# Optimization experiments

Hardware: AMD Instinct MI355X
Metric: run time of the kernel (lower is better)

Reference implementation:

```python
import jax, jax.numpy as jnp
import numpy as np

B, ENC, DEC, TSTEPS, PRED = 512, 2048, 1024, 12, 24
IN_DIM = ENC + 1 + TSTEPS  # 2061


def setup_inputs() -> dict:
    key = jax.random.key(0)
    ks = jax.random.split(key, 12)
    s = 0.05  # small init scale for numerical stability
    return {
        "encoder_out": jax.random.normal(ks[0], (B, ENC), jnp.float32),
        "oni_input": jax.random.normal(ks[1], (B, 1), jnp.float32),
        "ssi": jax.random.normal(ks[2], (B, TSTEPS), jnp.float32),
        "W_ih": jax.random.normal(ks[3], (4 * DEC, IN_DIM), jnp.float32) * s,
        "b_ih": jax.random.normal(ks[4], (4 * DEC,), jnp.float32) * s,
        "W_hh": jax.random.normal(ks[5], (4 * DEC, DEC), jnp.float32) * s,
        "b_hh": jax.random.normal(ks[6], (4 * DEC,), jnp.float32) * s,
        "W_l1": jax.random.normal(ks[7], (DEC, DEC * PRED), jnp.float32) * s,
        "b_l1": jax.random.normal(ks[8], (DEC,), jnp.float32) * s,
        "W_l2": jax.random.normal(ks[9], (DEC, DEC), jnp.float32) * s,
        "b_l2": jax.random.normal(ks[10], (DEC,), jnp.float32) * s,
    }


def reference(encoder_out, oni_input, ssi, W_ih, b_ih, W_hh, b_hh, W_l1, b_l1, W_l2, b_l2):
    # cfg.lstm=True, cfg.loss_criterion='enso', dropout p=0 (identity)
    x = jnp.concatenate([encoder_out, oni_input, ssi], axis=1)  # (B, IN_DIM)
    # input is identical every step: precompute input projection once
    x_proj = x @ W_ih.T + b_ih + b_hh  # (B, 4*DEC)
    D = W_hh.shape[1]
    T = W_l1.shape[1] // D
    b = x.shape[0]

    def step(carry, _):
        h, c = carry
        gates = x_proj + h @ W_hh.T  # (B, 4D), PyTorch gate order i,f,g,o
        i, f, g, o = jnp.split(gates, 4, axis=1)
        c = jax.nn.sigmoid(f) * c + jax.nn.sigmoid(i) * jnp.tanh(g)
        h = jax.nn.sigmoid(o) * jnp.tanh(c)
        return (h, c), h

    init = (jnp.zeros((b, D), x.dtype), jnp.zeros((b, D), x.dtype))
    _, hs = jax.lax.scan(step, init, None, length=T)  # (T, B, D)
    # torch.stack(dim=2) then flatten(start_dim=1) -> layout (B, D*T)
    preds = jnp.transpose(hs, (1, 2, 0)).reshape(b, D * T)
    preds = jax.nn.sigmoid(preds @ W_l1.T + b_l1)
    preds = preds @ W_l2.T + b_l2
    return jax.nn.sigmoid(preds)  # 'enso' head; dropout(p=0) is identity
```

## Files before the change

kernel.cpp:

```cpp
#include <hip/hip_runtime.h>
#include <hip/hip_bf16.h>

#define BSZ   512
#define ENCD  2048
#define DECD  1024
#define TST   12
#define PREDT 24
#define INDIM 2061
#define KPAD  2112
#define G4    4096
#define KH    24576

typedef __attribute__((ext_vector_type(8))) short s8v;
typedef __attribute__((ext_vector_type(4))) short s4v;
typedef __attribute__((ext_vector_type(4))) float f4v;

__device__ __forceinline__ short bf16_of(float f) {
  union { float f; unsigned u; } x; x.f = f;
  unsigned r = x.u + 0x7fffu + ((x.u >> 16) & 1u);
  return (short)(r >> 16);
}
__device__ __forceinline__ float sigf(float x) { return 1.f / (1.f + __expf(-x)); }
__device__ __forceinline__ float tanh_(float x) { return 1.f - 2.f / (1.f + __expf(2.f * x)); }

__device__ __forceinline__ int lds_off(int row, int colb) {
  return row * 128 + (colb ^ ((row & 7) << 4));
}


__global__ void prep_x(const float* __restrict__ enc, const float* __restrict__ oni,
                       const float* __restrict__ ssi, short* __restrict__ x_bf) {
  int idx = blockIdx.x * 256 + threadIdx.x;
  if (idx >= BSZ * KPAD) return;
  int b = idx / KPAD, k = idx % KPAD;
  float v = 0.f;
  if (k < ENCD) v = enc[b * ENCD + k];
  else if (k == ENCD) v = oni[b];
  else if (k < INDIM) v = ssi[b * TST + (k - ENCD - 1)];
  x_bf[idx] = bf16_of(v);
}

__global__ void prep_wih(const float* __restrict__ W, short* __restrict__ o) {
  int idx = blockIdx.x * 256 + threadIdx.x;
  int rp = idx / KPAD; int k = idx - rp * KPAD;
  int dblk = rp >> 6, rem = rp & 63, g = rem >> 4, dl = rem & 15;
  int srow = g * 1024 + dblk * 16 + dl;
  float v = (k < INDIM) ? W[(size_t)srow * INDIM + k] : 0.f;
  o[idx] = bf16_of(v);
}

__global__ void prep_whh(const float* __restrict__ W, short* __restrict__ o) {
  int idx = blockIdx.x * 256 + threadIdx.x;
  int rp = idx >> 10; int k = idx & 1023;
  int dblk = rp >> 6, rem = rp & 63, g = rem >> 4, dl = rem & 15;
  int srow = g * 1024 + dblk * 16 + dl;
  o[idx] = bf16_of(W[(size_t)srow * 1024 + k]);
}

__global__ __launch_bounds__(256, 1) void xproj_k(
    const short* __restrict__ x_bf, const short* __restrict__ wih_bf,
    const float* __restrict__ b_ih, const float* __restrict__ b_hh,
    float* __restrict__ xp_p) {
  __shared__ __align__(16) char sA[2][16384];
  __shared__ __align__(16) char sB[2][8192];
  int tid = threadIdx.x, lane = tid & 63, w = tid >> 6;
  int L = blockIdx.x;
  int bm = L >> 6, pb = (L & 7) * 8 + ((L >> 3) & 7);
  const int l4 = lane & 15, lg = lane >> 4;

  s8v aR[4], bR[2];
  auto LOAD = [&](int kt) {
    int kk = kt * 64;
#pragma unroll
    for (int i = 0; i < 4; ++i) {
      int c = tid + i * 256, r = c >> 3, sl = c & 7;
      aR[i] = *(const s8v*)(x_bf + (size_t)(bm * 128 + r) * KPAD + kk + sl * 8);
    }
#pragma unroll
    for (int i = 0; i < 2; ++i) {
      int c = tid + i * 256, r = c >> 3, sl = c & 7;
      bR[i] = *(const s8v*)(wih_bf + (size_t)(pb * 64 + r) * KPAD + kk + sl * 8);
    }
  };
  auto WRITE = [&](int buf) {
#pragma unroll
    for (int i = 0; i < 4; ++i) {
      int c = tid + i * 256, r = c >> 3, sl = c & 7;
      *(s8v*)(sA[buf] + lds_off(r, sl * 16)) = aR[i];
    }
#pragma unroll
    for (int i = 0; i < 2; ++i) {
      int c = tid + i * 256, r = c >> 3, sl = c & 7;
      *(s8v*)(sB[buf] + lds_off(r, sl * 16)) = bR[i];
    }
  };

  f4v acc[2][4] = {};
  LOAD(0); WRITE(0); LOAD(1);
  __syncthreads();
  for (int kt = 0; kt < 33; ++kt) {
    int cur = kt & 1;
    if (kt < 32) WRITE(cur ^ 1);
    if (kt < 31) LOAD(kt + 2);
#pragma unroll
    for (int ks = 0; ks < 2; ++ks) {
      int colb = ks * 64 + lg * 16;
      s8v af[2], bf[4];
#pragma unroll
      for (int mi = 0; mi < 2; ++mi)
        af[mi] = *(const s8v*)(sA[cur] + lds_off(w * 32 + mi * 16 + l4, colb));
#pragma unroll
      for (int ni = 0; ni < 4; ++ni)
        bf[ni] = *(const s8v*)(sB[cur] + lds_off(ni * 16 + l4, colb));
#pragma unroll
      for (int mi = 0; mi < 2; ++mi)
#pragma unroll
        for (int ni = 0; ni < 4; ++ni)
          acc[mi][ni] = __builtin_amdgcn_mfma_f32_16x16x32_bf16(af[mi], bf[ni], acc[mi][ni], 0, 0, 0);
    }
    __syncthreads();
  }
#pragma unroll
  for (int ni = 0; ni < 4; ++ni) {
    int src = ni * 1024 + pb * 16 + l4;
    float bv = b_ih[src] + b_hh[src];
#pragma unroll
    for (int mi = 0; mi < 2; ++mi)
#pragma unroll
      for (int j = 0; j < 4; ++j) {
        int row = bm * 128 + w * 32 + mi * 16 + lg * 4 + j;
        xp_p[(size_t)row * G4 + pb * 64 + ni * 16 + l4] = acc[mi][ni][j] + bv;
      }
  }
}

template <bool FIRST>
__global__ __launch_bounds__(256, 2) void step_k(
    const short* __restrict__ h_in, const short* __restrict__ whh_bf,
    const float* __restrict__ xp_p, float* __restrict__ c_st,
    short* __restrict__ h_out, short* __restrict__ hs_t, int tstep) {
  __shared__ __align__(16) char sB[2][8192];
  __shared__ __align__(16) char sA[4][2][4096];
  int tid = threadIdx.x, lane = tid & 63, w = tid >> 6;
  int cp = blockIdx.x, bm = blockIdx.y;
  const int l4 = lane & 15, lg = lane >> 4;
  const int d = cp * 16 + l4;

  float xg[2][4][4], cpre[2][4];
#pragma unroll
  for (int mi = 0; mi < 2; ++mi)
#pragma unroll
    for (int j = 0; j < 4; ++j) {
      int row = bm * 128 + w * 32 + mi * 16 + lg * 4 + j;
      size_t xb = (size_t)row * G4 + cp * 64 + l4;
      xg[mi][j][0] = xp_p[xb];
      xg[mi][j][1] = xp_p[xb + 16];
      xg[mi][j][2] = xp_p[xb + 32];
      xg[mi][j][3] = xp_p[xb + 48];
      cpre[mi][j] = FIRST ? 0.f : c_st[(size_t)row * DECD + d];
    }

  f4v acc[2][4] = {};

  if (!FIRST) {
    const short* bbase = whh_bf + (size_t)cp * 64 * DECD;
    const short* abase = h_in + (size_t)(bm * 128 + w * 32) * DECD;
    s8v aR[4], bR[2];
    auto LOAD = [&](int kt) {
      int kk = kt * 64;
#pragma unroll
      for (int i = 0; i < 4; ++i) {
        int c = lane + i * 64, r = c >> 3, sl = c & 7;
        aR[i] = *(const s8v*)(abase + (size_t)r * DECD + kk + sl * 8);
      }
#pragma unroll
      for (int i = 0; i < 2; ++i) {
        int c = tid + i * 256, r = c >> 3, sl = c & 7;
        bR[i] = *(const s8v*)(bbase + (size_t)r * DECD + kk + sl * 8);
      }
    };
    auto WRITE = [&](int buf) {
#pragma unroll
      for (int i = 0; i < 4; ++i) {
        int c = lane + i * 64, r = c >> 3, sl = c & 7;
        *(s8v*)(sA[w][buf] + lds_off(r, sl * 16)) = aR[i];
      }
#pragma unroll
      for (int i = 0; i < 2; ++i) {
        int c = tid + i * 256, r = c >> 3, sl = c & 7;
        *(s8v*)(sB[buf] + lds_off(r, sl * 16)) = bR[i];
      }
    };
    LOAD(0); WRITE(0); LOAD(1);
    __syncthreads();
    for (int kt = 0; kt < 16; ++kt) {
      int cur = kt & 1;
      if (kt < 15) WRITE(cur ^ 1);
      if (kt < 14) LOAD(kt + 2);
#pragma unroll
      for (int ks = 0; ks < 2; ++ks) {
        int colb = ks * 64 + lg * 16;
        s8v af[2], bf[4];
#pragma unroll
        for (int mi = 0; mi < 2; ++mi)
          af[mi] = *(const s8v*)(sA[w][cur] + lds_off(mi * 16 + l4, colb));
#pragma unroll
        for (int ni = 0; ni < 4; ++ni)
          bf[ni] = *(const s8v*)(sB[cur] + lds_off(ni * 16 + l4, colb));
#pragma unroll
        for (int mi = 0; mi < 2; ++mi)
#pragma unroll
          for (int ni = 0; ni < 4; ++ni)
            acc[mi][ni] = __builtin_amdgcn_mfma_f32_16x16x32_bf16(af[mi], bf[ni], acc[mi][ni], 0, 0, 0);
      }
      __syncthreads();
    }
  }

#pragma unroll
  for (int mi = 0; mi < 2; ++mi)
#pragma unroll
    for (int j = 0; j < 4; ++j) {
      int row = bm * 128 + w * 32 + mi * 16 + lg * 4 + j;
      float gi = xg[mi][j][0] + acc[mi][0][j];
      float gf = xg[mi][j][1] + acc[mi][1][j];
      float gg = xg[mi][j][2] + acc[mi][2][j];
      float go = xg[mi][j][3] + acc[mi][3][j];
      float cn = sigf(gf) * cpre[mi][j] + sigf(gi) * tanh_(gg);
      float h = sigf(go) * tanh_(cn);
      size_t cd = (size_t)row * DECD + d;
      c_st[cd] = cn;
      short hb = bf16_of(h);
      if (tstep < 23) h_out[cd] = hb;
      hs_t[(size_t)tstep * (BSZ * DECD) + cd] = hb;
    }
}

__global__ void transpose_k(const short* __restrict__ hs_t, short* __restrict__ hs) {
  int g = blockIdx.x * 256 + threadIdx.x;
  int row = g >> 10, d = g & 1023;
#pragma unroll
  for (int i = 0; i < 3; ++i) {
    s8v v;
#pragma unroll
    for (int u = 0; u < 8; ++u)
      v[u] = hs_t[(size_t)(i * 8 + u) * (BSZ * DECD) + (size_t)row * DECD + d];
    *(s8v*)(hs + (size_t)row * KH + d * PREDT + i * 8) = v;
  }
}

template <int EPI>
__global__ __launch_bounds__(256, 2) void gemm2_k(
    const short* __restrict__ A, int lda, const float* __restrict__ Bw, int ldb,
    int ntiles, int kchunk, const float* __restrict__ bias1,
    float* __restrict__ Cf, int ldc) {
  __shared__ __align__(16) char sA[2][16384];
  __shared__ __align__(16) char sB[2][16384];
  int tid = threadIdx.x, lane = tid & 63, wid = tid >> 6;
  int wr = wid >> 1, wc = wid & 1, l4 = lane & 15, lg = lane >> 4;
  int bn = blockIdx.x * 128, bm = blockIdx.y * 128;
  int k0 = blockIdx.z * kchunk;
  size_t zoff = (size_t)blockIdx.z * BSZ * (size_t)ldc;
  s8v aR[4]; f4v bR[4][2];
  auto LOAD = [&](int kt) {
    int kk = k0 + kt * 64;
#pragma unroll
    for (int i = 0; i < 4; ++i) {
      int c = tid + i * 256, r = c >> 3, sl = c & 7;
      aR[i] = *(const s8v*)(A + (size_t)(bm + r) * lda + kk + sl * 8);
      const float* src = Bw + (size_t)(bn + r) * ldb + kk + sl * 8;
      bR[i][0] = *(const f4v*)src;
      bR[i][1] = *(const f4v*)(src + 4);
    }
  };
  auto WRITE = [&](int buf) {
#pragma unroll
    for (int i = 0; i < 4; ++i) {
      int c = tid + i * 256, r = c >> 3, sl = c & 7;
      *(s8v*)(sA[buf] + lds_off(r, sl * 16)) = aR[i];
      s8v v;
#pragma unroll
      for (int j = 0; j < 4; ++j) { v[j] = bf16_of(bR[i][0][j]); v[4 + j] = bf16_of(bR[i][1][j]); }
      *(s8v*)(sB[buf] + lds_off(r, sl * 16)) = v;
    }
  };
  f4v acc[4][4] = {};
  LOAD(0); WRITE(0);
  if (ntiles > 1) LOAD(1);
  __syncthreads();
  for (int kt = 0; kt < ntiles; ++kt) {
    int cur = kt & 1;
    if (kt + 1 < ntiles) WRITE(cur ^ 1);
    if (kt + 2 < ntiles) LOAD(kt + 2);
#pragma unroll
    for (int ks = 0; ks < 2; ++ks) {
      int colb = ks * 64 + lg * 16;
      s8v af[4], bf[4];
#pragma unroll
      for (int mi = 0; mi < 4; ++mi)
        af[mi] = *(const s8v*)(sA[cur] + lds_off(wr * 64 + mi * 16 + l4, colb));
#pragma unroll
      for (int ni = 0; ni < 4; ++ni)
        bf[ni] = *(const s8v*)(sB[cur] + lds_off(wc * 64 + ni * 16 + l4, colb));
#pragma unroll
      for (int mi = 0; mi < 4; ++mi)
#pragma unroll
        for (int ni = 0; ni < 4; ++ni)
          acc[mi][ni] = __builtin_amdgcn_mfma_f32_16x16x32_bf16(af[mi], bf[ni], acc[mi][ni], 0, 0, 0);
    }
    __syncthreads();
  }
#pragma unroll
  for (int mi = 0; mi < 4; ++mi)
#pragma unroll
    for (int ni = 0; ni < 4; ++ni)
#pragma unroll
      for (int j = 0; j < 4; ++j) {
        int row = bm + wr * 64 + mi * 16 + lg * 4 + j;
        int col = bn + wc * 64 + ni * 16 + l4;
        float v = acc[mi][ni][j];
        if (EPI == 1) Cf[zoff + (size_t)row * ldc + col] = v;
        else Cf[(size_t)row * ldc + col] = sigf(v + bias1[col]);
      }
}

__global__ void reduce16(const float* __restrict__ part, const float* __restrict__ b_l1,
                         short* __restrict__ z1) {
  int i4 = blockIdx.x * 256 + threadIdx.x;
  int base = i4 * 4;
  int n = base & (DECD - 1);
  f4v s = *(const f4v*)(b_l1 + n);
#pragma unroll
  for (int z = 0; z < 16; ++z) {
    f4v p = *(const f4v*)(part + (size_t)z * (BSZ * DECD) + base);
#pragma unroll
    for (int j = 0; j < 4; ++j) s[j] += p[j];
  }
  s4v o;
#pragma unroll
  for (int j = 0; j < 4; ++j) o[j] = bf16_of(sigf(s[j]));
  *(s4v*)(z1 + base) = o;
}


extern "C" void kernel_launch(void* const* d_in, const int* in_sizes, int n_in,
                              void* d_out, int out_size, void* d_ws, size_t ws_size,
                              hipStream_t stream) {
  const float* enc  = (const float*)d_in[0];
  const float* oni  = (const float*)d_in[1];
  const float* ssi  = (const float*)d_in[2];
  const float* W_ih = (const float*)d_in[3];
  const float* b_ih = (const float*)d_in[4];
  const float* W_hh = (const float*)d_in[5];
  const float* b_hh = (const float*)d_in[6];
  const float* W_l1 = (const float*)d_in[7];
  const float* b_l1 = (const float*)d_in[8];
  const float* W_l2 = (const float*)d_in[9];
  const float* b_l2 = (const float*)d_in[10];
  float* out = (float*)d_out;
  (void)in_sizes; (void)n_in; (void)out_size; (void)ws_size;

  char* ws = (char*)d_ws;
  size_t off = 0;
  auto carve = [&](size_t bytes) { char* p = ws + off; off += (bytes + 255) & ~(size_t)255; return p; };
  short* x_bf   = (short*)carve((size_t)BSZ * KPAD * 2);
  short* wih_bf = (short*)carve((size_t)G4 * KPAD * 2);
  short* whh_bf = (short*)carve((size_t)G4 * DECD * 2);
  float* xp_p   = (float*)carve((size_t)BSZ * G4 * 4);
  short* h0     = (short*)carve((size_t)BSZ * DECD * 2);
  short* h1     = (short*)carve((size_t)BSZ * DECD * 2);
  float* c_st   = (float*)carve((size_t)BSZ * DECD * 4);
  float* part   = (float*)ws;
  if (off < (size_t)16 * BSZ * DECD * 4) off = (((size_t)16 * BSZ * DECD * 4) + 255) & ~(size_t)255;
  short* hs_t   = (short*)carve((size_t)PREDT * BSZ * DECD * 2);
  short* hs     = (short*)carve((size_t)BSZ * KH * 2);
  short* z1     = (short*)carve((size_t)BSZ * DECD * 2);

  prep_x  <<<(BSZ * KPAD) / 256, 256, 0, stream>>>(enc, oni, ssi, x_bf);
  prep_wih<<<(G4 * KPAD) / 256, 256, 0, stream>>>(W_ih, wih_bf);
  prep_whh<<<(G4 * DECD) / 256, 256, 0, stream>>>(W_hh, whh_bf);

  xproj_k<<<256, 256, 0, stream>>>(x_bf, wih_bf, b_ih, b_hh, xp_p);

  step_k<true><<<dim3(64, 4), 256, 0, stream>>>(nullptr, whh_bf, xp_p, c_st, h0, hs_t, 0);
  for (int t = 1; t < PREDT; ++t) {
    short* hr = (t & 1) ? h0 : h1;
    short* hw = (t & 1) ? h1 : h0;
    step_k<false><<<dim3(64, 4), 256, 0, stream>>>(hr, whh_bf, xp_p, c_st, hw, hs_t, t);
  }

  transpose_k<<<(BSZ * DECD) / 256, 256, 0, stream>>>(hs_t, hs);

  gemm2_k<1><<<dim3(8, 4, 16), 256, 0, stream>>>(hs, KH, W_l1, KH, 24, KH / 16, nullptr, part, DECD);
  reduce16<<<(BSZ * DECD) / 1024, 256, 0, stream>>>(part, b_l1, z1);

  gemm2_k<2><<<dim3(8, 4, 1), 256, 0, stream>>>(z1, DECD, W_l2, DECD, 16, DECD, b_l2, out, DECD);
}
```

Measured before the change: 412.6 us.

## Fuse W_ih conversion into xproj, write hs directly, shrink GEMM M tile

Removes the separate prep_wih kernel: xproj now reads fp32 W_ih directly with row remapping and converts to bf16 in registers, zero-padding past the input dimension. The step kernel writes hidden states straight into the interleaved (B, D*T) layout, which removes the hs_t buffer and the transpose kernel. The final GEMMs use a 64-row M tile with launch bounds allowing 3 blocks, doubling grid size for better occupancy. The trade-offs are scattered 2-byte strided stores in each step kernel and redundant fp32 weight reads and conversion in xproj.

New measurement: 487.5 us. 18.2% more time.

```diff
diff --git a/kernel.cpp b/kernel.cpp
--- a/kernel.cpp
+++ b/kernel.cpp
@@ -40,15 +40,6 @@
   x_bf[idx] = bf16_of(v);
 }
 
-__global__ void prep_wih(const float* __restrict__ W, short* __restrict__ o) {
-  int idx = blockIdx.x * 256 + threadIdx.x;
-  int rp = idx / KPAD; int k = idx - rp * KPAD;
-  int dblk = rp >> 6, rem = rp & 63, g = rem >> 4, dl = rem & 15;
-  int srow = g * 1024 + dblk * 16 + dl;
-  float v = (k < INDIM) ? W[(size_t)srow * INDIM + k] : 0.f;
-  o[idx] = bf16_of(v);
-}
-
 __global__ void prep_whh(const float* __restrict__ W, short* __restrict__ o) {
   int idx = blockIdx.x * 256 + threadIdx.x;
   int rp = idx >> 10; int k = idx & 1023;
@@ -58,7 +49,7 @@
 }
 
 __global__ __launch_bounds__(256, 1) void xproj_k(
-    const short* __restrict__ x_bf, const short* __restrict__ wih_bf,
+    const short* __restrict__ x_bf, const float* __restrict__ W_ih,
     const float* __restrict__ b_ih, const float* __restrict__ b_hh,
     float* __restrict__ xp_p) {
   __shared__ __align__(16) char sA[2][16384];
@@ -79,7 +70,20 @@
 #pragma unroll
     for (int i = 0; i < 2; ++i) {
       int c = tid + i * 256, r = c >> 3, sl = c & 7;
-      bR[i] = *(const s8v*)(wih_bf + (size_t)(pb * 64 + r) * KPAD + kk + sl * 8);
+      int srow = (r >> 4) * 1024 + pb * 16 + (r & 15);
+      const float* src = W_ih + (size_t)srow * INDIM + kk + sl * 8;
+      if (kt < 32) {
+        f4v f0 = *(const f4v*)src;
+        f4v f1 = *(const f4v*)(src + 4);
+#pragma unroll
+        for (int j = 0; j < 4; ++j) { bR[i][j] = bf16_of(f0[j]); bR[i][4 + j] = bf16_of(f1[j]); }
+      } else {
+#pragma unroll
+        for (int j = 0; j < 8; ++j) {
+          int kg = kk + sl * 8 + j;
+          bR[i][j] = (kg < INDIM) ? bf16_of(src[j]) : (short)0;
+        }
+      }
     }
   };
   auto WRITE = [&](int buf) {
@@ -138,7 +142,7 @@
 __global__ __launch_bounds__(256, 2) void step_k(
     const short* __restrict__ h_in, const short* __restrict__ whh_bf,
     const float* __restrict__ xp_p, float* __restrict__ c_st,
-    short* __restrict__ h_out, short* __restrict__ hs_t, int tstep) {
+    short* __restrict__ h_out, short* __restrict__ hs, int tstep) {
   __shared__ __align__(16) char sB[2][8192];
   __shared__ __align__(16) char sA[4][2][4096];
   int tid = threadIdx.x, lane = tid & 63, w = tid >> 6;
@@ -232,42 +236,33 @@
       c_st[cd] = cn;
       short hb = bf16_of(h);
       if (tstep < 23) h_out[cd] = hb;
-      hs_t[(size_t)tstep * (BSZ * DECD) + cd] = hb;
-    }
-}
-
-__global__ void transpose_k(const short* __restrict__ hs_t, short* __restrict__ hs) {
-  int g = blockIdx.x * 256 + threadIdx.x;
-  int row = g >> 10, d = g & 1023;
-#pragma unroll
-  for (int i = 0; i < 3; ++i) {
-    s8v v;
-#pragma unroll
-    for (int u = 0; u < 8; ++u)
-      v[u] = hs_t[(size_t)(i * 8 + u) * (BSZ * DECD) + (size_t)row * DECD + d];
-    *(s8v*)(hs + (size_t)row * KH + d * PREDT + i * 8) = v;
-  }
+      hs[(size_t)row * KH + d * PREDT + tstep] = hb;
+    }
 }
 
 template <int EPI>
-__global__ __launch_bounds__(256, 2) void gemm2_k(
+__global__ __launch_bounds__(256, 3) void gemm3_k(
     const short* __restrict__ A, int lda, const float* __restrict__ Bw, int ldb,
     int ntiles, int kchunk, const float* __restrict__ bias1,
     float* __restrict__ Cf, int ldc) {
-  __shared__ __align__(16) char sA[2][16384];
+  __shared__ __align__(16) char sA[2][8192];
   __shared__ __align__(16) char sB[2][16384];
   int tid = threadIdx.x, lane = tid & 63, wid = tid >> 6;
   int wr = wid >> 1, wc = wid & 1, l4 = lane & 15, lg = lane >> 4;
-  int bn = blockIdx.x * 128, bm = blockIdx.y * 128;
+  int bn = blockIdx.x * 128, bm = blockIdx.y * 64;
   int k0 = blockIdx.z * kchunk;
   size_t zoff = (size_t)blockIdx.z * BSZ * (size_t)ldc;
-  s8v aR[4]; f4v bR[4][2];
+  s8v aR[2]; f4v bR[4][2];
   auto LOAD = [&](int kt) {
     int kk = k0 + kt * 64;
 #pragma unroll
+    for (int i = 0; i < 2; ++i) {
+      int c = tid + i * 256, r = c >> 3, sl = c & 7;
+      aR[i] = *(const s8v*)(A + (size_t)(bm + r) * lda + kk + sl * 8);
+    }
+#pragma unroll
     for (int i = 0; i < 4; ++i) {
       int c = tid + i * 256, r = c >> 3, sl = c & 7;
-      aR[i] = *(const s8v*)(A + (size_t)(bm + r) * lda + kk + sl * 8);
       const float* src = Bw + (size_t)(bn + r) * ldb + kk + sl * 8;
       bR[i][0] = *(const f4v*)src;
       bR[i][1] = *(const f4v*)(src + 4);
@@ -275,16 +270,20 @@
   };
   auto WRITE = [&](int buf) {
 #pragma unroll
+    for (int i = 0; i < 2; ++i) {
+      int c = tid + i * 256, r = c >> 3, sl = c & 7;
+      *(s8v*)(sA[buf] + lds_off(r, sl * 16)) = aR[i];
+    }
+#pragma unroll
     for (int i = 0; i < 4; ++i) {
       int c = tid + i * 256, r = c >> 3, sl = c & 7;
-      *(s8v*)(sA[buf] + lds_off(r, sl * 16)) = aR[i];
       s8v v;
 #pragma unroll
       for (int j = 0; j < 4; ++j) { v[j] = bf16_of(bR[i][0][j]); v[4 + j] = bf16_of(bR[i][1][j]); }
       *(s8v*)(sB[buf] + lds_off(r, sl * 16)) = v;
     }
   };
-  f4v acc[4][4] = {};
+  f4v acc[2][4] = {};
   LOAD(0); WRITE(0);
   if (ntiles > 1) LOAD(1);
   __syncthreads();
@@ -295,15 +294,15 @@
 #pragma unroll
     for (int ks = 0; ks < 2; ++ks) {
       int colb = ks * 64 + lg * 16;
-      s8v af[4], bf[4];
-#pragma unroll
-      for (int mi = 0; mi < 4; ++mi)
-        af[mi] = *(const s8v*)(sA[cur] + lds_off(wr * 64 + mi * 16 + l4, colb));
+      s8v af[2], bf[4];
+#pragma unroll
+      for (int mi = 0; mi < 2; ++mi)
+        af[mi] = *(const s8v*)(sA[cur] + lds_off(wr * 32 + mi * 16 + l4, colb));
 #pragma unroll
       for (int ni = 0; ni < 4; ++ni)
         bf[ni] = *(const s8v*)(sB[cur] + lds_off(wc * 64 + ni * 16 + l4, colb));
 #pragma unroll
-      for (int mi = 0; mi < 4; ++mi)
+      for (int mi = 0; mi < 2; ++mi)
 #pragma unroll
         for (int ni = 0; ni < 4; ++ni)
           acc[mi][ni] = __builtin_amdgcn_mfma_f32_16x16x32_bf16(af[mi], bf[ni], acc[mi][ni], 0, 0, 0);
@@ -311,12 +310,12 @@
     __syncthreads();
   }
 #pragma unroll
-  for (int mi = 0; mi < 4; ++mi)
+  for (int mi = 0; mi < 2; ++mi)
 #pragma unroll
     for (int ni = 0; ni < 4; ++ni)
 #pragma unroll
       for (int j = 0; j < 4; ++j) {
-        int row = bm + wr * 64 + mi * 16 + lg * 4 + j;
+        int row = bm + wr * 32 + mi * 16 + lg * 4 + j;
         int col = bn + wc * 64 + ni * 16 + l4;
         float v = acc[mi][ni][j];
         if (EPI == 1) Cf[zoff + (size_t)row * ldc + col] = v;
@@ -364,7 +363,6 @@
   size_t off = 0;
   auto carve = [&](size_t bytes) { char* p = ws + off; off += (bytes + 255) & ~(size_t)255; return p; };
   short* x_bf   = (short*)carve((size_t)BSZ * KPAD * 2);
-  short* wih_bf = (short*)carve((size_t)G4 * KPAD * 2);
   short* whh_bf = (short*)carve((size_t)G4 * DECD * 2);
   float* xp_p   = (float*)carve((size_t)BSZ * G4 * 4);
   short* h0     = (short*)carve((size_t)BSZ * DECD * 2);
@@ -372,27 +370,23 @@
   float* c_st   = (float*)carve((size_t)BSZ * DECD * 4);
   float* part   = (float*)ws;
   if (off < (size_t)16 * BSZ * DECD * 4) off = (((size_t)16 * BSZ * DECD * 4) + 255) & ~(size_t)255;
-  short* hs_t   = (short*)carve((size_t)PREDT * BSZ * DECD * 2);
   short* hs     = (short*)carve((size_t)BSZ * KH * 2);
   short* z1     = (short*)carve((size_t)BSZ * DECD * 2);
 
   prep_x  <<<(BSZ * KPAD) / 256, 256, 0, stream>>>(enc, oni, ssi, x_bf);
-  prep_wih<<<(G4 * KPAD) / 256, 256, 0, stream>>>(W_ih, wih_bf);
   prep_whh<<<(G4 * DECD) / 256, 256, 0, stream>>>(W_hh, whh_bf);
 
-  xproj_k<<<256, 256, 0, stream>>>(x_bf, wih_bf, b_ih, b_hh, xp_p);
-
-  step_k<true><<<dim3(64, 4), 256, 0, stream>>>(nullptr, whh_bf, xp_p, c_st, h0, hs_t, 0);
+  xproj_k<<<256, 256, 0, stream>>>(x_bf, W_ih, b_ih, b_hh, xp_p);
+
+  step_k<true><<<dim3(64, 4), 256, 0, stream>>>(nullptr, whh_bf, xp_p, c_st, h0, hs, 0);
   for (int t = 1; t < PREDT; ++t) {
     short* hr = (t & 1) ? h0 : h1;
     short* hw = (t & 1) ? h1 : h0;
-    step_k<false><<<dim3(64, 4), 256, 0, stream>>>(hr, whh_bf, xp_p, c_st, hw, hs_t, t);
-  }
-
-  transpose_k<<<(BSZ * DECD) / 256, 256, 0, stream>>>(hs_t, hs);
-
-  gemm2_k<1><<<dim3(8, 4, 16), 256, 0, stream>>>(hs, KH, W_l1, KH, 24, KH / 16, nullptr, part, DECD);
+    step_k<false><<<dim3(64, 4), 256, 0, stream>>>(hr, whh_bf, xp_p, c_st, hw, hs, t);
+  }
+
+  gemm3_k<1><<<dim3(8, 8, 16), 256, 0, stream>>>(hs, KH, W_l1, KH, 24, KH / 16, nullptr, part, DECD);
   reduce16<<<(BSZ * DECD) / 1024, 256, 0, stream>>>(part, b_l1, z1);
 
-  gemm2_k<2><<<dim3(8, 4, 1), 256, 0, stream>>>(z1, DECD, W_l2, DECD, 16, DECD, b_l2, out, DECD);
-}
+  gemm3_k<2><<<dim3(8, 8, 1), 256, 0, stream>>>(z1, DECD, W_l2, DECD, 16, DECD, b_l2, out, DECD);
+}
```

## Fuse W_ih conversion into xproj and overlap W_l1 bf16 conversion with LSTM steps

Applied to the files above, without the earlier changes.

Drops the separate prep_wih kernel: xproj now reads fp32 W_ih directly, converts it to bf16 in registers and handles the K-tail with guarded loads. The 24 latency-bound LSTM step launches each get an extra row of blocks that converts a slice of W_l1 to bf16, hiding that conversion inside steps that leave the GPU underused. The large GEMM then reads bf16 weights, halving its weight traffic. The h ping-pong buffers are removed and steps read the previous h from hs_t. This costs extra workspace, with a fallback path when the workspace is too small, and adds unaligned float4 loads on W_ih rows since the row stride of 2061 is odd.

After: 507.1 us. 1.23x slower.

```diff
diff --git a/kernel.cpp b/kernel.cpp
--- a/kernel.cpp
+++ b/kernel.cpp
@@ -40,15 +40,6 @@
   x_bf[idx] = bf16_of(v);
 }
 
-__global__ void prep_wih(const float* __restrict__ W, short* __restrict__ o) {
-  int idx = blockIdx.x * 256 + threadIdx.x;
-  int rp = idx / KPAD; int k = idx - rp * KPAD;
-  int dblk = rp >> 6, rem = rp & 63, g = rem >> 4, dl = rem & 15;
-  int srow = g * 1024 + dblk * 16 + dl;
-  float v = (k < INDIM) ? W[(size_t)srow * INDIM + k] : 0.f;
-  o[idx] = bf16_of(v);
-}
-
 __global__ void prep_whh(const float* __restrict__ W, short* __restrict__ o) {
   int idx = blockIdx.x * 256 + threadIdx.x;
   int rp = idx >> 10; int k = idx & 1023;
@@ -58,7 +49,7 @@
 }
 
 __global__ __launch_bounds__(256, 1) void xproj_k(
-    const short* __restrict__ x_bf, const short* __restrict__ wih_bf,
+    const short* __restrict__ x_bf, const float* __restrict__ W_ih,
     const float* __restrict__ b_ih, const float* __restrict__ b_hh,
     float* __restrict__ xp_p) {
   __shared__ __align__(16) char sA[2][16384];
@@ -79,7 +70,20 @@
 #pragma unroll
     for (int i = 0; i < 2; ++i) {
       int c = tid + i * 256, r = c >> 3, sl = c & 7;
-      bR[i] = *(const s8v*)(wih_bf + (size_t)(pb * 64 + r) * KPAD + kk + sl * 8);
+      int srow = (r >> 4) * 1024 + pb * 16 + (r & 15);
+      const float* src = W_ih + (size_t)srow * INDIM + kk + sl * 8;
+      if (kt < 32) {
+        f4v f0 = *(const f4v*)src;
+        f4v f1 = *(const f4v*)(src + 4);
+#pragma unroll
+        for (int j = 0; j < 4; ++j) { bR[i][j] = bf16_of(f0[j]); bR[i][4 + j] = bf16_of(f1[j]); }
+      } else {
+#pragma unroll
+        for (int j = 0; j < 8; ++j) {
+          int kg = kk + sl * 8 + j;
+          bR[i][j] = (kg < INDIM) ? bf16_of(src[j]) : (short)0;
+        }
+      }
     }
   };
   auto WRITE = [&](int buf) {
@@ -134,14 +138,29 @@
   }
 }
 
-template <bool FIRST>
+template <bool FIRST, bool CONV>
 __global__ __launch_bounds__(256, 2) void step_k(
-    const short* __restrict__ h_in, const short* __restrict__ whh_bf,
-    const float* __restrict__ xp_p, float* __restrict__ c_st,
-    short* __restrict__ h_out, short* __restrict__ hs_t, int tstep) {
+    const short* __restrict__ whh_bf, const float* __restrict__ xp_p,
+    float* __restrict__ c_st, short* __restrict__ hs_t, int tstep,
+    const float* __restrict__ wl1, short* __restrict__ wl1b) {
   __shared__ __align__(16) char sB[2][8192];
   __shared__ __align__(16) char sA[4][2][4096];
   int tid = threadIdx.x, lane = tid & 63, w = tid >> 6;
+
+  if (CONV && blockIdx.y == 4) {
+    size_t base = (size_t)tstep * 1048576 + (size_t)(blockIdx.x * 256 + tid) * 64;
+#pragma unroll
+    for (int i = 0; i < 8; ++i) {
+      f4v f0 = *(const f4v*)(wl1 + base + i * 8);
+      f4v f1 = *(const f4v*)(wl1 + base + i * 8 + 4);
+      s8v v;
+#pragma unroll
+      for (int j = 0; j < 4; ++j) { v[j] = bf16_of(f0[j]); v[4 + j] = bf16_of(f1[j]); }
+      *(s8v*)(wl1b + base + i * 8) = v;
+    }
+    return;
+  }
+
   int cp = blockIdx.x, bm = blockIdx.y;
   const int l4 = lane & 15, lg = lane >> 4;
   const int d = cp * 16 + l4;
@@ -163,6 +182,7 @@
   f4v acc[2][4] = {};
 
   if (!FIRST) {
+    const short* h_in = hs_t + (size_t)(tstep - 1) * (BSZ * DECD);
     const short* bbase = whh_bf + (size_t)cp * 64 * DECD;
     const short* abase = h_in + (size_t)(bm * 128 + w * 32) * DECD;
     s8v aR[4], bR[2];
@@ -217,6 +237,7 @@
     }
   }
 
+  short* hw = hs_t + (size_t)tstep * (BSZ * DECD);
 #pragma unroll
   for (int mi = 0; mi < 2; ++mi)
 #pragma unroll
@@ -230,9 +251,7 @@
       float h = sigf(go) * tanh_(cn);
       size_t cd = (size_t)row * DECD + d;
       c_st[cd] = cn;
-      short hb = bf16_of(h);
-      if (tstep < 23) h_out[cd] = hb;
-      hs_t[(size_t)tstep * (BSZ * DECD) + cd] = hb;
+      hw[cd] = bf16_of(h);
     }
 }
 
@@ -249,9 +268,10 @@
   }
 }
 
-template <int EPI>
+template <int EPI, bool BF16B>
 __global__ __launch_bounds__(256, 2) void gemm2_k(
-    const short* __restrict__ A, int lda, const float* __restrict__ Bw, int ldb,
+    const short* __restrict__ A, int lda, const short* __restrict__ Bb,
+    const float* __restrict__ Bf, int ldb,
     int ntiles, int kchunk, const float* __restrict__ bias1,
     float* __restrict__ Cf, int ldc) {
   __shared__ __align__(16) char sA[2][16384];
@@ -261,16 +281,20 @@
   int bn = blockIdx.x * 128, bm = blockIdx.y * 128;
   int k0 = blockIdx.z * kchunk;
   size_t zoff = (size_t)blockIdx.z * BSZ * (size_t)ldc;
-  s8v aR[4]; f4v bR[4][2];
+  s8v aR[4], bB[4]; f4v bR[4][2];
   auto LOAD = [&](int kt) {
     int kk = k0 + kt * 64;
 #pragma unroll
     for (int i = 0; i < 4; ++i) {
       int c = tid + i * 256, r = c >> 3, sl = c & 7;
       aR[i] = *(const s8v*)(A + (size_t)(bm + r) * lda + kk + sl * 8);
-      const float* src = Bw + (size_t)(bn + r) * ldb + kk + sl * 8;
-      bR[i][0] = *(const f4v*)src;
-      bR[i][1] = *(const f4v*)(src + 4);
+      if (BF16B) {
+        bB[i] = *(const s8v*)(Bb + (size_t)(bn + r) * ldb + kk + sl * 8);
+      } else {
+        const float* src = Bf + (size_t)(bn + r) * ldb + kk + sl * 8;
+        bR[i][0] = *(const f4v*)src;
+        bR[i][1] = *(const f4v*)(src + 4);
+      }
     }
   };
   auto WRITE = [&](int buf) {
@@ -278,10 +302,14 @@
     for (int i = 0; i < 4; ++i) {
       int c = tid + i * 256, r = c >> 3, sl = c & 7;
       *(s8v*)(sA[buf] + lds_off(r, sl * 16)) = aR[i];
-      s8v v;
-#pragma unroll
-      for (int j = 0; j < 4; ++j) { v[j] = bf16_of(bR[i][0][j]); v[4 + j] = bf16_of(bR[i][1][j]); }
-      *(s8v*)(sB[buf] + lds_off(r, sl * 16)) = v;
+      if (BF16B) {
+        *(s8v*)(sB[buf] + lds_off(r, sl * 16)) = bB[i];
+      } else {
+        s8v v;
+#pragma unroll
+        for (int j = 0; j < 4; ++j) { v[j] = bf16_of(bR[i][0][j]); v[4 + j] = bf16_of(bR[i][1][j]); }
+        *(s8v*)(sB[buf] + lds_off(r, sl * 16)) = v;
+      }
     }
   };
   f4v acc[4][4] = {};
@@ -358,41 +386,47 @@
   const float* W_l2 = (const float*)d_in[9];
   const float* b_l2 = (const float*)d_in[10];
   float* out = (float*)d_out;
-  (void)in_sizes; (void)n_in; (void)out_size; (void)ws_size;
+  (void)in_sizes; (void)n_in; (void)out_size;
 
   char* ws = (char*)d_ws;
   size_t off = 0;
   auto carve = [&](size_t bytes) { char* p = ws + off; off += (bytes + 255) & ~(size_t)255; return p; };
   short* x_bf   = (short*)carve((size_t)BSZ * KPAD * 2);
-  short* wih_bf = (short*)carve((size_t)G4 * KPAD * 2);
   short* whh_bf = (short*)carve((size_t)G4 * DECD * 2);
   float* xp_p   = (float*)carve((size_t)BSZ * G4 * 4);
-  short* h0     = (short*)carve((size_t)BSZ * DECD * 2);
-  short* h1     = (short*)carve((size_t)BSZ * DECD * 2);
   float* c_st   = (float*)carve((size_t)BSZ * DECD * 4);
   float* part   = (float*)ws;
   if (off < (size_t)16 * BSZ * DECD * 4) off = (((size_t)16 * BSZ * DECD * 4) + 255) & ~(size_t)255;
   short* hs_t   = (short*)carve((size_t)PREDT * BSZ * DECD * 2);
   short* hs     = (short*)carve((size_t)BSZ * KH * 2);
   short* z1     = (short*)carve((size_t)BSZ * DECD * 2);
+  size_t off_no_wl1b = off;
+  short* wl1b   = (short*)carve((size_t)DECD * KH * 2);
+  const bool big = ws_size >= off;
+  (void)off_no_wl1b;
 
   prep_x  <<<(BSZ * KPAD) / 256, 256, 0, stream>>>(enc, oni, ssi, x_bf);
-  prep_wih<<<(G4 * KPAD) / 256, 256, 0, stream>>>(W_ih, wih_bf);
   prep_whh<<<(G4 * DECD) / 256, 256, 0, stream>>>(W_hh, whh_bf);
 
-  xproj_k<<<256, 256, 0, stream>>>(x_bf, wih_bf, b_ih, b_hh, xp_p);
-
-  step_k<true><<<dim3(64, 4), 256, 0, stream>>>(nullptr, whh_bf, xp_p, c_st, h0, hs_t, 0);
-  for (int t = 1; t < PREDT; ++t) {
-    short* hr = (t & 1) ? h0 : h1;
-    short* hw = (t & 1) ? h1 : h0;
-    step_k<false><<<dim3(64, 4), 256, 0, stream>>>(hr, whh_bf, xp_p, c_st, hw, hs_t, t);
+  xproj_k<<<256, 256, 0, stream>>>(x_bf, W_ih, b_ih, b_hh, xp_p);
+
+  if (big) {
+    step_k<true, true><<<dim3(64, 5), 256, 0, stream>>>(whh_bf, xp_p, c_st, hs_t, 0, W_l1, wl1b);
+    for (int t = 1; t < PREDT; ++t)
+      step_k<false, true><<<dim3(64, 5), 256, 0, stream>>>(whh_bf, xp_p, c_st, hs_t, t, W_l1, wl1b);
+  } else {
+    step_k<true, false><<<dim3(64, 4), 256, 0, stream>>>(whh_bf, xp_p, c_st, hs_t, 0, nullptr, nullptr);
+    for (int t = 1; t < PREDT; ++t)
+      step_k<false, false><<<dim3(64, 4), 256, 0, stream>>>(whh_bf, xp_p, c_st, hs_t, t, nullptr, nullptr);
   }
 
   transpose_k<<<(BSZ * DECD) / 256, 256, 0, stream>>>(hs_t, hs);
 
-  gemm2_k<1><<<dim3(8, 4, 16), 256, 0, stream>>>(hs, KH, W_l1, KH, 24, KH / 16, nullptr, part, DECD);
+  if (big)
+    gemm2_k<1, true><<<dim3(8, 4, 16), 256, 0, stream>>>(hs, KH, wl1b, nullptr, KH, 24, KH / 16, nullptr, part, DECD);
+  else
+    gemm2_k<1, false><<<dim3(8, 4, 16), 256, 0, stream>>>(hs, KH, nullptr, W_l1, KH, 24, KH / 16, nullptr, part, DECD);
   reduce16<<<(BSZ * DECD) / 1024, 256, 0, stream>>>(part, b_l1, z1);
 
-  gemm2_k<2><<<dim3(8, 4, 1), 256, 0, stream>>>(z1, DECD, W_l2, DECD, 16, DECD, b_l2, out, DECD);
-}
+  gemm2_k<2, false><<<dim3(8, 4, 1), 256, 0, stream>>>(z1, DECD, nullptr, W_l2, DECD, 16, DECD, b_l2, out, DECD);
+}
```

## Split LSTM step blocks to 64 rows and load h fragments directly to registers

Applied to the files above, without the earlier changes.

The recurrent step kernel now uses 128-thread blocks covering 64 batch rows, which doubles the grid to 512 blocks so more CUs have work on a latency-bound step. The A operand (hidden state) is no longer staged through LDS. Each wave loads its MFMA fragments straight from global memory into registers, double-buffered across k-tiles, with the loop unrolled in pairs. This removes the LDS writes and reads for h and cuts LDS use per block. In exchange, each W_hh tile is now fetched by twice as many blocks, and the direct global loads of A fragments may coalesce less well.

After: 504.5 us. +22.3%, slower.

```diff
diff --git a/kernel.cpp b/kernel.cpp
--- a/kernel.cpp
+++ b/kernel.cpp
@@ -135,23 +135,23 @@
 }
 
 template <bool FIRST>
-__global__ __launch_bounds__(256, 2) void step_k(
+__global__ __launch_bounds__(128) void step_k(
     const short* __restrict__ h_in, const short* __restrict__ whh_bf,
     const float* __restrict__ xp_p, float* __restrict__ c_st,
     short* __restrict__ h_out, short* __restrict__ hs_t, int tstep) {
   __shared__ __align__(16) char sB[2][8192];
-  __shared__ __align__(16) char sA[4][2][4096];
   int tid = threadIdx.x, lane = tid & 63, w = tid >> 6;
   int cp = blockIdx.x, bm = blockIdx.y;
   const int l4 = lane & 15, lg = lane >> 4;
   const int d = cp * 16 + l4;
+  const int rbase = bm * 64 + w * 32;
 
   float xg[2][4][4], cpre[2][4];
 #pragma unroll
   for (int mi = 0; mi < 2; ++mi)
 #pragma unroll
     for (int j = 0; j < 4; ++j) {
-      int row = bm * 128 + w * 32 + mi * 16 + lg * 4 + j;
+      int row = rbase + mi * 16 + lg * 4 + j;
       size_t xb = (size_t)row * G4 + cp * 64 + l4;
       xg[mi][j][0] = xp_p[xb];
       xg[mi][j][1] = xp_p[xb + 16];
@@ -164,46 +164,41 @@
 
   if (!FIRST) {
     const short* bbase = whh_bf + (size_t)cp * 64 * DECD;
-    const short* abase = h_in + (size_t)(bm * 128 + w * 32) * DECD;
-    s8v aR[4], bR[2];
-    auto LOAD = [&](int kt) {
+    const short* abase = h_in + (size_t)rbase * DECD;
+    s8v bR[4];
+    auto LOADB = [&](int kt) {
       int kk = kt * 64;
 #pragma unroll
       for (int i = 0; i < 4; ++i) {
-        int c = lane + i * 64, r = c >> 3, sl = c & 7;
-        aR[i] = *(const s8v*)(abase + (size_t)r * DECD + kk + sl * 8);
-      }
-#pragma unroll
-      for (int i = 0; i < 2; ++i) {
-        int c = tid + i * 256, r = c >> 3, sl = c & 7;
+        int c = tid + i * 128, r = c >> 3, sl = c & 7;
         bR[i] = *(const s8v*)(bbase + (size_t)r * DECD + kk + sl * 8);
       }
     };
-    auto WRITE = [&](int buf) {
+    auto WRITEB = [&](int buf) {
 #pragma unroll
       for (int i = 0; i < 4; ++i) {
-        int c = lane + i * 64, r = c >> 3, sl = c & 7;
-        *(s8v*)(sA[w][buf] + lds_off(r, sl * 16)) = aR[i];
-      }
-#pragma unroll
-      for (int i = 0; i < 2; ++i) {
-        int c = tid + i * 256, r = c >> 3, sl = c & 7;
+        int c = tid + i * 128, r = c >> 3, sl = c & 7;
         *(s8v*)(sB[buf] + lds_off(r, sl * 16)) = bR[i];
       }
     };
-    LOAD(0); WRITE(0); LOAD(1);
-    __syncthreads();
-    for (int kt = 0; kt < 16; ++kt) {
+    s8v a0[2][2], a1[2][2];
+    auto LOADA = [&](int kt, s8v (&af)[2][2]) {
+      int kk = kt * 64;
+#pragma unroll
+      for (int mi = 0; mi < 2; ++mi)
+#pragma unroll
+        for (int ks = 0; ks < 2; ++ks)
+          af[mi][ks] = *(const s8v*)(abase + (size_t)(mi * 16 + l4) * DECD + kk + ks * 32 + lg * 8);
+    };
+    auto PHASE = [&](int kt, s8v (&aC)[2][2], s8v (&aN)[2][2]) {
       int cur = kt & 1;
-      if (kt < 15) WRITE(cur ^ 1);
-      if (kt < 14) LOAD(kt + 2);
+      if (kt < 15) WRITEB(cur ^ 1);
+      if (kt < 14) LOADB(kt + 2);
+      if (kt < 15) LOADA(kt + 1, aN);
 #pragma unroll
       for (int ks = 0; ks < 2; ++ks) {
         int colb = ks * 64 + lg * 16;
-        s8v af[2], bf[4];
-#pragma unroll
-        for (int mi = 0; mi < 2; ++mi)
-          af[mi] = *(const s8v*)(sA[w][cur] + lds_off(mi * 16 + l4, colb));
+        s8v bf[4];
 #pragma unroll
         for (int ni = 0; ni < 4; ++ni)
           bf[ni] = *(const s8v*)(sB[cur] + lds_off(ni * 16 + l4, colb));
@@ -211,9 +206,16 @@
         for (int mi = 0; mi < 2; ++mi)
 #pragma unroll
           for (int ni = 0; ni < 4; ++ni)
-            acc[mi][ni] = __builtin_amdgcn_mfma_f32_16x16x32_bf16(af[mi], bf[ni], acc[mi][ni], 0, 0, 0);
+            acc[mi][ni] = __builtin_amdgcn_mfma_f32_16x16x32_bf16(aC[mi][ks], bf[ni], acc[mi][ni], 0, 0, 0);
       }
       __syncthreads();
+    };
+    LOADB(0); WRITEB(0); LOADB(1); LOADA(0, a0);
+    __syncthreads();
+#pragma unroll
+    for (int k2 = 0; k2 < 8; ++k2) {
+      PHASE(2 * k2, a0, a1);
+      PHASE(2 * k2 + 1, a1, a0);
     }
   }
 
@@ -221,7 +223,7 @@
   for (int mi = 0; mi < 2; ++mi)
 #pragma unroll
     for (int j = 0; j < 4; ++j) {
-      int row = bm * 128 + w * 32 + mi * 16 + lg * 4 + j;
+      int row = rbase + mi * 16 + lg * 4 + j;
       float gi = xg[mi][j][0] + acc[mi][0][j];
       float gf = xg[mi][j][1] + acc[mi][1][j];
       float gg = xg[mi][j][2] + acc[mi][2][j];
@@ -382,11 +384,11 @@
 
   xproj_k<<<256, 256, 0, stream>>>(x_bf, wih_bf, b_ih, b_hh, xp_p);
 
-  step_k<true><<<dim3(64, 4), 256, 0, stream>>>(nullptr, whh_bf, xp_p, c_st, h0, hs_t, 0);
+  step_k<true><<<dim3(64, 8), 128, 0, stream>>>(nullptr, whh_bf, xp_p, c_st, h0, hs_t, 0);
   for (int t = 1; t < PREDT; ++t) {
     short* hr = (t & 1) ? h0 : h1;
     short* hw = (t & 1) ? h1 : h0;
-    step_k<false><<<dim3(64, 4), 256, 0, stream>>>(hr, whh_bf, xp_p, c_st, hw, hs_t, t);
+    step_k<false><<<dim3(64, 8), 128, 0, stream>>>(hr, whh_bf, xp_p, c_st, hw, hs_t, t);
   }
 
   transpose_k<<<(BSZ * DECD) / 256, 256, 0, stream>>>(hs_t, hs);
```
